# Optimization experiments

Hardware: AMD Instinct MI355X
Metric: run time of the kernel (lower is better)

## Reference

```python
import jax, jax.numpy as jnp
import numpy as np

TEMPERATURE = 5.0

def setup_inputs() -> dict:
    key = jax.random.key(0)
    k1, k2 = jax.random.split(key)
    B, D = 8192, 128
    features = jax.random.normal(k1, (B, D), dtype=jnp.float32)
    labels = jax.random.randint(k2, (B,), 0, 100, dtype=jnp.int64)
    return {"features": features, "labels": labels, "fac_label": 3}


def reference(features, labels, fac_label):
    # features: [B, D], labels: [B]
    B = features.shape[0]
    # positive-pair mask; note original's mask_scale row-copy loop is a no-op,
    # so mask_scale == mask, and mask_cross_feature == ones (fac_label unused in effect)
    mask = (labels[:, None] == labels[None, :]).astype(features.dtype)  # [B, B]

    sim = jnp.matmul(features, features.T) / TEMPERATURE  # [B, B]
    logits_max = jax.lax.stop_gradient(jnp.max(sim, axis=1, keepdims=True))
    logits = sim - logits_max

    # remove self-contrast (diagonal)
    logits_mask = 1.0 - jnp.eye(B, dtype=features.dtype)
    mask = mask * logits_mask

    exp_logits = jnp.exp(logits) * logits_mask
    log_prob = logits - jnp.log(1e-12 + exp_logits.sum(axis=1, keepdims=True))

    mean_log_prob_pos_mask = (mask * log_prob).sum(axis=1)  # [B]
    # vectorized form of the per-element reciprocal loop: 1/count where count>0 else 0
    cnt = mask.sum(axis=1)
    recip = jnp.where(cnt == 0, 0.0, 1.0 / jnp.where(cnt == 0, 1.0, cnt))

    loss = -(mean_log_prob_pos_mask * recip).mean()
    return loss
```

## Files before the change

kernel.cpp:

```cpp
#include <hip/hip_runtime.h>


#define BN 8192
#define DK 128
#define INV_T 0.2f

#define CHUNKS 8
#define CHUNK_COLS (BN / CHUNKS)
#define ROWS_PER_BLOCK 128
#define RT_PER_WAVE 2

typedef __attribute__((ext_vector_type(8))) short bf16x8;
typedef __attribute__((ext_vector_type(4))) float f32x4;

__device__ __forceinline__ unsigned short f2bf(float f) {
    unsigned u = __builtin_bit_cast(unsigned, f);
    u += 0x7fffu + ((u >> 16) & 1u);
    return (unsigned short)(u >> 16);
}

__global__ __launch_bounds__(256) void cast_kernel(const float* __restrict__ F,
                                                   unsigned short* __restrict__ Fb) {
    int idx = blockIdx.x * 256 + threadIdx.x;
    float4 v = ((const float4*)F)[idx];
    ushort4 o;
    o.x = f2bf(v.x); o.y = f2bf(v.y); o.z = f2bf(v.z); o.w = f2bf(v.w);
    ((ushort4*)Fb)[idx] = o;
}

__global__ __launch_bounds__(256) void supcon_main(const short* __restrict__ Fb,
                                                   const int* __restrict__ labels,
                                                   float4* __restrict__ part) {
    const int t    = threadIdx.x;
    const int wave = t >> 6;
    const int lane = t & 63;
    const int quad = lane >> 4;
    const int l16  = lane & 15;
    const int rowBase = blockIdx.x * ROWS_PER_BLOCK + wave * (RT_PER_WAVE * 16);
    const int colBase = blockIdx.y * CHUNK_COLS;

    bf16x8 a[RT_PER_WAVE][4];
#pragma unroll
    for (int rt = 0; rt < RT_PER_WAVE; ++rt)
#pragma unroll
        for (int kt = 0; kt < 4; ++kt)
            a[rt][kt] = *(const bf16x8*)(Fb + (size_t)(rowBase + rt * 16 + l16) * DK
                                            + kt * 32 + quad * 8);

    int   rlbl[RT_PER_WAVE][4], irow[RT_PER_WAVE][4];
    float m[RT_PER_WAVE][4], Z[RT_PER_WAVE][4], A[RT_PER_WAVE][4], C[RT_PER_WAVE][4];
#pragma unroll
    for (int rt = 0; rt < RT_PER_WAVE; ++rt)
#pragma unroll
        for (int r = 0; r < 4; ++r) {
            irow[rt][r] = rowBase + rt * 16 + quad * 4 + r;
            rlbl[rt][r] = labels[irow[rt][r]];
            m[rt][r] = -__builtin_inff();
            Z[rt][r] = 0.f; A[rt][r] = 0.f; C[rt][r] = 0.f;
        }

    for (int jt = 0; jt < CHUNK_COLS / 16; ++jt) {
        const int j0 = colBase + jt * 16;
        bf16x8 b[4];
#pragma unroll
        for (int kt = 0; kt < 4; ++kt)
            b[kt] = *(const bf16x8*)(Fb + (size_t)(j0 + l16) * DK + kt * 32 + quad * 8);
        const int jcol = j0 + l16;
        const int clbl = labels[jcol];

#pragma unroll
        for (int rt = 0; rt < RT_PER_WAVE; ++rt) {
            f32x4 acc = {0.f, 0.f, 0.f, 0.f};
#pragma unroll
            for (int kt = 0; kt < 4; ++kt)
                acc = __builtin_amdgcn_mfma_f32_16x16x32_bf16(a[rt][kt], b[kt], acc, 0, 0, 0);

#pragma unroll
            for (int r = 0; r < 4; ++r) {
                float s    = acc[r] * INV_T;
                bool  diag = (jcol == irow[rt][r]);
                float mo   = m[rt][r];
                float mn   = fmaxf(mo, s);
                float zs   = Z[rt][r];
                if (mn > mo) zs *= __expf(mo - mn);
                float e = __expf(s - mn);
                zs += diag ? 0.f : e;
                Z[rt][r] = zs;
                m[rt][r] = mn;
                bool match = (!diag) && (clbl == rlbl[rt][r]);
                A[rt][r] += match ? s : 0.f;
                C[rt][r] += match ? 1.f : 0.f;
            }
        }
    }

#pragma unroll
    for (int rt = 0; rt < RT_PER_WAVE; ++rt)
#pragma unroll
        for (int r = 0; r < 4; ++r) {
            float mm = m[rt][r], zz = Z[rt][r], aa = A[rt][r], cc = C[rt][r];
#pragma unroll
            for (int h = 1; h < 16; h <<= 1) {
                float om = __shfl_xor(mm, h);
                float oz = __shfl_xor(zz, h);
                float oa = __shfl_xor(aa, h);
                float oc = __shfl_xor(cc, h);
                float mn = fmaxf(mm, om);
                zz = zz * __expf(mm - mn) + oz * __expf(om - mn);
                mm = mn; aa += oa; cc += oc;
            }
            if (l16 == 0)
                part[(size_t)blockIdx.y * BN + irow[rt][r]] = make_float4(mm, zz, aa, cc);
        }
}

__global__ __launch_bounds__(256) void supcon_finalize(const float4* __restrict__ part,
                                                       float* __restrict__ bsums) {
    const int i = blockIdx.x * 256 + threadIdx.x;
    float mm = -__builtin_inff(), zz = 0.f, aa = 0.f, cc = 0.f;
#pragma unroll
    for (int c = 0; c < CHUNKS; ++c) {
        float4 p = part[(size_t)c * BN + i];
        float mn = fmaxf(mm, p.x);
        zz = zz * __expf(mm - mn) + p.y * __expf(p.x - mn);
        mm = mn; aa += p.z; cc += p.w;
    }
    float term = 0.f;
    if (cc > 0.5f) term = (aa - cc * mm) / cc - __logf(1e-12f + zz);

    float sum = term;
#pragma unroll
    for (int h = 1; h < 64; h <<= 1) sum += __shfl_xor(sum, h);
    __shared__ float ss[4];
    if ((threadIdx.x & 63) == 0) ss[threadIdx.x >> 6] = sum;
    __syncthreads();
    if (threadIdx.x == 0) bsums[blockIdx.x] = ss[0] + ss[1] + ss[2] + ss[3];
}

__global__ void supcon_final(const float* __restrict__ bsums, float* __restrict__ out) {
    float v = (threadIdx.x < 32) ? bsums[threadIdx.x] : 0.f;
#pragma unroll
    for (int h = 1; h < 64; h <<= 1) v += __shfl_xor(v, h);
    if (threadIdx.x == 0) out[0] = -v * (1.0f / BN);
}

extern "C" void kernel_launch(void* const* d_in, const int* in_sizes, int n_in,
                              void* d_out, int out_size, void* d_ws, size_t ws_size,
                              hipStream_t stream) {
    const float* F      = (const float*)d_in[0];
    const int*   labels = (const int*)d_in[1];
    float* out = (float*)d_out;
    char*  ws  = (char*)d_ws;

    unsigned short* Fb   = (unsigned short*)ws;
    float4*         part = (float4*)(ws + (size_t)2 * 1024 * 1024);
    float*          bsum = (float*)(ws + (size_t)3 * 1024 * 1024);

    cast_kernel<<<(BN * DK / 4) / 256, 256, 0, stream>>>(F, Fb);
    supcon_main<<<dim3(BN / ROWS_PER_BLOCK, CHUNKS), 256, 0, stream>>>((const short*)Fb,
                                                                       labels, part);
    supcon_finalize<<<BN / 256, 256, 0, stream>>>(part, bsum);
    supcon_final<<<1, 64, 0, stream>>>(bsum, out);
}
```

Baseline: 129.3 us.

## Reformulate SupCon with class-sum positives, fixed diagonal shift, and fused ticket finalize

```diff
diff --git a/kernel.cpp b/kernel.cpp
--- a/kernel.cpp
+++ b/kernel.cpp
@@ -3,15 +3,27 @@
 
 #define BN 8192
 #define DK 128
+#define NCLS 128
 #define INV_T 0.2f
-
-#define CHUNKS 8
-#define CHUNK_COLS (BN / CHUNKS)
-#define ROWS_PER_BLOCK 128
-#define RT_PER_WAVE 2
+#define LOG2E 1.4426950408889634f
+
+#define GX 32
+#define GY 16
+#define CHUNK_COLS (BN / GY)
 
 typedef __attribute__((ext_vector_type(8))) short bf16x8;
 typedef __attribute__((ext_vector_type(4))) float f32x4;
+
+#define OFF_FB   0
+#define OFF_SII  (BN * DK * 2)
+#define OFF_ZERO (OFF_SII + BN * 4)
+#define OFF_G    OFF_ZERO
+#define OFF_CNT  (OFF_G + NCLS * DK * 4)
+#define OFF_Z    (OFF_CNT + 512)
+#define OFF_RA   (OFF_Z + BN * 4)
+#define OFF_TKT  (OFF_RA + BN * 4)
+#define OFF_MISC (OFF_TKT + GX * 4)
+#define ZERO_BYTES (OFF_MISC + 128 - OFF_ZERO)
 
 __device__ __forceinline__ unsigned short f2bf(float f) {
     unsigned u = __builtin_bit_cast(unsigned, f);
@@ -19,45 +31,95 @@
     return (unsigned short)(u >> 16);
 }
 
-__global__ __launch_bounds__(256) void cast_kernel(const float* __restrict__ F,
-                                                   unsigned short* __restrict__ Fb) {
-    int idx = blockIdx.x * 256 + threadIdx.x;
+__global__ __launch_bounds__(256) void supcon_prep(const float* __restrict__ F,
+                                                   const int* __restrict__ labels,
+                                                   unsigned short* __restrict__ Fb,
+                                                   float* __restrict__ sii,
+                                                   float* __restrict__ g,
+                                                   int* __restrict__ counts) {
+    const int idx = blockIdx.x * 256 + threadIdx.x;
+    const int row = idx >> 5;
+    const int d0  = (idx & 31) * 4;
     float4 v = ((const float4*)F)[idx];
+
     ushort4 o;
     o.x = f2bf(v.x); o.y = f2bf(v.y); o.z = f2bf(v.z); o.w = f2bf(v.w);
     ((ushort4*)Fb)[idx] = o;
-}
-
-__global__ __launch_bounds__(256) void supcon_main(const short* __restrict__ Fb,
-                                                   const int* __restrict__ labels,
-                                                   float4* __restrict__ part) {
-    const int t    = threadIdx.x;
-    const int wave = t >> 6;
-    const int lane = t & 63;
-    const int quad = lane >> 4;
-    const int l16  = lane & 15;
-    const int rowBase = blockIdx.x * ROWS_PER_BLOCK + wave * (RT_PER_WAVE * 16);
-    const int colBase = blockIdx.y * CHUNK_COLS;
-
-    bf16x8 a[RT_PER_WAVE][4];
-#pragma unroll
-    for (int rt = 0; rt < RT_PER_WAVE; ++rt)
+
+    const int lbl = labels[row];
+    unsafeAtomicAdd(&g[lbl * DK + d0 + 0], v.x);
+    unsafeAtomicAdd(&g[lbl * DK + d0 + 1], v.y);
+    unsafeAtomicAdd(&g[lbl * DK + d0 + 2], v.z);
+    unsafeAtomicAdd(&g[lbl * DK + d0 + 3], v.w);
+
+    float sq = v.x * v.x + v.y * v.y + v.z * v.z + v.w * v.w;
+    sq += __shfl_xor(sq, 1);  sq += __shfl_xor(sq, 2);  sq += __shfl_xor(sq, 4);
+    sq += __shfl_xor(sq, 8);  sq += __shfl_xor(sq, 16);
+    if ((threadIdx.x & 31) == 0) {
+        sii[row] = sq * INV_T;
+        atomicAdd(&counts[lbl], 1);
+    }
+}
+
+__global__ __launch_bounds__(256) void supcon_main(
+    const short* __restrict__ Fb, const float* __restrict__ F,
+    const int* __restrict__ labels, const float* __restrict__ sii,
+    const float* __restrict__ g, const int* __restrict__ counts,
+    float* __restrict__ Zrow, float* __restrict__ rowA,
+    int* __restrict__ rbTicket, int* __restrict__ gTicket,
+    float* __restrict__ lossAcc, float* __restrict__ out)
+{
+    const int tid  = threadIdx.x;
+    const int wave = tid >> 6, lane = tid & 63;
+    const int quad = lane >> 4, l16 = lane & 15;
+    const int bx = blockIdx.x, by = blockIdx.y;
+    const int rowBase = bx * 256 + wave * 64;
+    const int colBase = by * CHUNK_COLS;
+
+    __shared__ int   tkt;
+    __shared__ float ss[4];
+
+    if (by == 0) {
+        const int r0  = bx * 256 + tid;
+        const int lbl = labels[r0];
+        const float c = (float)(counts[lbl] - 1);
+        if (c > 0.5f) {
+            const float4* fr = (const float4*)(F + (size_t)r0 * DK);
+            const float4* gr = (const float4*)(g + (size_t)lbl * DK);
+            float dot = 0.f;
+#pragma unroll
+            for (int d = 0; d < DK / 4; ++d) {
+                float4 a = fr[d], b = gr[d];
+                dot += a.x * b.x + a.y * b.y + a.z * b.z + a.w * b.w;
+            }
+            const float s2 = sii[r0];
+            const float A  = dot * INV_T - s2;
+            unsafeAtomicAdd(&rowA[r0], (A - c * s2) / c);
+        }
+    }
+
+    bf16x8 a[4][4];
+#pragma unroll
+    for (int rt = 0; rt < 4; ++rt)
 #pragma unroll
         for (int kt = 0; kt < 4; ++kt)
             a[rt][kt] = *(const bf16x8*)(Fb + (size_t)(rowBase + rt * 16 + l16) * DK
                                             + kt * 32 + quad * 8);
 
-    int   rlbl[RT_PER_WAVE][4], irow[RT_PER_WAVE][4];
-    float m[RT_PER_WAVE][4], Z[RT_PER_WAVE][4], A[RT_PER_WAVE][4], C[RT_PER_WAVE][4];
-#pragma unroll
-    for (int rt = 0; rt < RT_PER_WAVE; ++rt)
-#pragma unroll
-        for (int r = 0; r < 4; ++r) {
-            irow[rt][r] = rowBase + rt * 16 + quad * 4 + r;
-            rlbl[rt][r] = labels[irow[rt][r]];
-            m[rt][r] = -__builtin_inff();
-            Z[rt][r] = 0.f; A[rt][r] = 0.f; C[rt][r] = 0.f;
-        }
+    float nc2[4][4];
+#pragma unroll
+    for (int rt = 0; rt < 4; ++rt)
+#pragma unroll
+        for (int r = 0; r < 4; ++r)
+            nc2[rt][r] = -sii[rowBase + rt * 16 + quad * 4 + r] * LOG2E;
+
+    float Z[4][4];
+#pragma unroll
+    for (int rt = 0; rt < 4; ++rt)
+#pragma unroll
+        for (int r = 0; r < 4; ++r) Z[rt][r] = 0.f;
+
+    const float K2 = INV_T * LOG2E;
 
     for (int jt = 0; jt < CHUNK_COLS / 16; ++jt) {
         const int j0 = colBase + jt * 16;
@@ -65,83 +127,56 @@
 #pragma unroll
         for (int kt = 0; kt < 4; ++kt)
             b[kt] = *(const bf16x8*)(Fb + (size_t)(j0 + l16) * DK + kt * 32 + quad * 8);
-        const int jcol = j0 + l16;
-        const int clbl = labels[jcol];
-
-#pragma unroll
-        for (int rt = 0; rt < RT_PER_WAVE; ++rt) {
+
+#pragma unroll
+        for (int rt = 0; rt < 4; ++rt) {
             f32x4 acc = {0.f, 0.f, 0.f, 0.f};
 #pragma unroll
             for (int kt = 0; kt < 4; ++kt)
                 acc = __builtin_amdgcn_mfma_f32_16x16x32_bf16(a[rt][kt], b[kt], acc, 0, 0, 0);
 
+            const bool dt = (j0 == rowBase + rt * 16);
 #pragma unroll
             for (int r = 0; r < 4; ++r) {
-                float s    = acc[r] * INV_T;
-                bool  diag = (jcol == irow[rt][r]);
-                float mo   = m[rt][r];
-                float mn   = fmaxf(mo, s);
-                float zs   = Z[rt][r];
-                if (mn > mo) zs *= __expf(mo - mn);
-                float e = __expf(s - mn);
-                zs += diag ? 0.f : e;
-                Z[rt][r] = zs;
-                m[rt][r] = mn;
-                bool match = (!diag) && (clbl == rlbl[rt][r]);
-                A[rt][r] += match ? s : 0.f;
-                C[rt][r] += match ? 1.f : 0.f;
+                float e = __builtin_amdgcn_exp2f(fmaf(acc[r], K2, nc2[rt][r]));
+                if (dt && (l16 == quad * 4 + r)) e = 0.f;
+                Z[rt][r] += e;
             }
         }
     }
 
 #pragma unroll
-    for (int rt = 0; rt < RT_PER_WAVE; ++rt)
+    for (int rt = 0; rt < 4; ++rt)
 #pragma unroll
         for (int r = 0; r < 4; ++r) {
-            float mm = m[rt][r], zz = Z[rt][r], aa = A[rt][r], cc = C[rt][r];
-#pragma unroll
-            for (int h = 1; h < 16; h <<= 1) {
-                float om = __shfl_xor(mm, h);
-                float oz = __shfl_xor(zz, h);
-                float oa = __shfl_xor(aa, h);
-                float oc = __shfl_xor(cc, h);
-                float mn = fmaxf(mm, om);
-                zz = zz * __expf(mm - mn) + oz * __expf(om - mn);
-                mm = mn; aa += oa; cc += oc;
-            }
+            float z = Z[rt][r];
+            z += __shfl_xor(z, 1); z += __shfl_xor(z, 2);
+            z += __shfl_xor(z, 4); z += __shfl_xor(z, 8);
             if (l16 == 0)
-                part[(size_t)blockIdx.y * BN + irow[rt][r]] = make_float4(mm, zz, aa, cc);
-        }
-}
-
-__global__ __launch_bounds__(256) void supcon_finalize(const float4* __restrict__ part,
-                                                       float* __restrict__ bsums) {
-    const int i = blockIdx.x * 256 + threadIdx.x;
-    float mm = -__builtin_inff(), zz = 0.f, aa = 0.f, cc = 0.f;
-#pragma unroll
-    for (int c = 0; c < CHUNKS; ++c) {
-        float4 p = part[(size_t)c * BN + i];
-        float mn = fmaxf(mm, p.x);
-        zz = zz * __expf(mm - mn) + p.y * __expf(p.x - mn);
-        mm = mn; aa += p.z; cc += p.w;
-    }
-    float term = 0.f;
-    if (cc > 0.5f) term = (aa - cc * mm) / cc - __logf(1e-12f + zz);
-
-    float sum = term;
-#pragma unroll
-    for (int h = 1; h < 64; h <<= 1) sum += __shfl_xor(sum, h);
-    __shared__ float ss[4];
-    if ((threadIdx.x & 63) == 0) ss[threadIdx.x >> 6] = sum;
+                unsafeAtomicAdd(&Zrow[rowBase + rt * 16 + quad * 4 + r], z);
+        }
+
     __syncthreads();
-    if (threadIdx.x == 0) bsums[blockIdx.x] = ss[0] + ss[1] + ss[2] + ss[3];
-}
-
-__global__ void supcon_final(const float* __restrict__ bsums, float* __restrict__ out) {
-    float v = (threadIdx.x < 32) ? bsums[threadIdx.x] : 0.f;
-#pragma unroll
-    for (int h = 1; h < 64; h <<= 1) v += __shfl_xor(v, h);
-    if (threadIdx.x == 0) out[0] = -v * (1.0f / BN);
+    if (tid == 0) { __threadfence(); tkt = atomicAdd(&rbTicket[bx], 1); }
+    __syncthreads();
+    if (tkt == GY - 1) {
+        const int i  = bx * 256 + tid;
+        const float Zv = unsafeAtomicAdd(&Zrow[i], 0.f);
+        const float Av = unsafeAtomicAdd(&rowA[i], 0.f);
+        const int   c  = counts[labels[i]] - 1;
+        float term = (c > 0) ? (Av - __logf(1e-12f + Zv)) : 0.f;
+#pragma unroll
+        for (int h = 1; h < 64; h <<= 1) term += __shfl_xor(term, h);
+        if (lane == 0) ss[wave] = term;
+        __syncthreads();
+        if (tid == 0) {
+            unsafeAtomicAdd(lossAcc, ss[0] + ss[1] + ss[2] + ss[3]);
+            __threadfence();
+            const int gt = atomicAdd(gTicket, 1);
+            if (gt == GX - 1)
+                out[0] = -unsafeAtomicAdd(lossAcc, 0.f) * (1.0f / BN);
+        }
+    }
 }
 
 extern "C" void kernel_launch(void* const* d_in, const int* in_sizes, int n_in,
@@ -152,13 +187,19 @@
     float* out = (float*)d_out;
     char*  ws  = (char*)d_ws;
 
-    unsigned short* Fb   = (unsigned short*)ws;
-    float4*         part = (float4*)(ws + (size_t)2 * 1024 * 1024);
-    float*          bsum = (float*)(ws + (size_t)3 * 1024 * 1024);
-
-    cast_kernel<<<(BN * DK / 4) / 256, 256, 0, stream>>>(F, Fb);
-    supcon_main<<<dim3(BN / ROWS_PER_BLOCK, CHUNKS), 256, 0, stream>>>((const short*)Fb,
-                                                                       labels, part);
-    supcon_finalize<<<BN / 256, 256, 0, stream>>>(part, bsum);
-    supcon_final<<<1, 64, 0, stream>>>(bsum, out);
-}
+    unsigned short* Fb     = (unsigned short*)(ws + OFF_FB);
+    float*          sii    = (float*)(ws + OFF_SII);
+    float*          g      = (float*)(ws + OFF_G);
+    int*            counts = (int*)(ws + OFF_CNT);
+    float*          Zrow   = (float*)(ws + OFF_Z);
+    float*          rowA   = (float*)(ws + OFF_RA);
+    int*            rbTkt  = (int*)(ws + OFF_TKT);
+    int*            gTkt   = (int*)(ws + OFF_MISC);
+    float*          lossA  = (float*)(ws + OFF_MISC + 4);
+
+    (void)hipMemsetAsync(ws + OFF_ZERO, 0, ZERO_BYTES, stream);
+    supcon_prep<<<BN * DK / 4 / 256, 256, 0, stream>>>(F, labels, Fb, sii, g, counts);
+    supcon_main<<<dim3(GX, GY), 256, 0, stream>>>((const short*)Fb, F, labels, sii,
+                                                  g, counts, Zrow, rowA,
+                                                  rbTkt, gTkt, lossA, out);
+}
```

Result: slower. 152.0 us (+17.6%).
